# Optimization experiments

Hardware: AMD Instinct MI355X
Metric: run time of the kernel (lower is better)

Reference implementation:

```python
import jax, jax.numpy as jnp
import numpy as np

B, L, V, E, H, C, OUT = 128, 256, 50000, 300, 128, 4, 2
D = 2 * H  # features_size == sequence_max_len (required by the conv kernel width)
FS = (2, 3, 4, 5)


def _p(key, shape, s=0.05):
    return (jax.random.normal(key, shape) * s).astype(jnp.float32)


def setup_inputs() -> dict:
    key = jax.random.key(0)
    ks = jax.random.split(key, 32)
    emb = _p(ks[0], (V, E)).at[0].set(0.0)  # padding_idx=0
    inp = {
        'utterance': jax.random.randint(ks[1], (B, L), 1, V, dtype=jnp.int32),
        'seq_lengths': jnp.full((B,), L, dtype=jnp.int32),
        'emb': emb,
        'w_ih0': _p(ks[2], (2, 3 * H, E)), 'w_hh0': _p(ks[3], (2, 3 * H, H)),
        'b_ih0': _p(ks[4], (2, 3 * H)), 'b_hh0': _p(ks[5], (2, 3 * H)),
        'w_ih1': _p(ks[6], (2, 3 * H, 2 * H)), 'w_hh1': _p(ks[7], (2, 3 * H, H)),
        'b_ih1': _p(ks[8], (2, 3 * H)), 'b_hh1': _p(ks[9], (2, 3 * H)),
        'att_w': _p(ks[10], (C, D, D)), 'att_b': _p(ks[11], (C,)),
        'att_wv2': _p(ks[12], (C, D, D)), 'att_bv': _p(ks[13], (C, D)),
        'att_wv1': _p(ks[14], (C, D)),
        'fc_w': _p(ks[15], (OUT, sum(FS))), 'fc_b': _p(ks[16], (OUT,)),
    }
    for i, fs in enumerate(FS):
        inp[f'conv_w{i}'] = _p(ks[17 + 2 * i], (fs, C, fs, L))
        inp[f'conv_b{i}'] = _p(ks[18 + 2 * i], (fs,))
    return inp


def _gru_dir(x, w_ih, w_hh, b_ih, b_hh, reverse):
    # x: (B,T,in) -> (B,T,H); PyTorch GRU cell equations, eval mode (no dropout)
    gx = jnp.einsum('bti,gi->btg', x, w_ih) + b_ih  # (B,T,3H)

    def step(h, gxt):
        gh = h @ w_hh.T + b_hh
        xr, xz, xn = jnp.split(gxt, 3, axis=-1)
        hr, hz, hn = jnp.split(gh, 3, axis=-1)
        r = jax.nn.sigmoid(xr + hr)
        z = jax.nn.sigmoid(xz + hz)
        n = jnp.tanh(xn + r * hn)
        h = (1.0 - z) * n + z * h
        return h, h

    h0 = jnp.zeros((x.shape[0], w_hh.shape[1]), x.dtype)
    _, ys = jax.lax.scan(step, h0, jnp.swapaxes(gx, 0, 1), reverse=reverse)
    return jnp.swapaxes(ys, 0, 1)


def _bigru_layer(x, w_ih, w_hh, b_ih, b_hh):
    f = _gru_dir(x, w_ih[0], w_hh[0], b_ih[0], b_hh[0], False)
    b = _gru_dir(x, w_ih[1], w_hh[1], b_ih[1], b_hh[1], True)
    return jnp.concatenate([f, b], axis=-1)


def _forward(utterance, emb, w_ih0, w_hh0, b_ih0, b_hh0, w_ih1, w_hh1, b_ih1, b_hh1,
             att_w, att_b, att_wv2, att_bv, att_wv1, conv_params, fc_w, fc_b):
    x = emb[utterance]                                   # (B,L,E)
    x = _bigru_layer(x, w_ih0, w_hh0, b_ih0, b_hh0)      # (B,L,2H)
    x = _bigru_layer(x, w_ih1, w_hh1, b_ih1, b_hh1)      # (B,L,D)
    # --- AMCNN attention, vectorized over channels c ---
    mat = jnp.einsum('bld,cde->cble', x, att_w)          # mat_l per channel (C,B,L,D)
    # M_l[b,i,j] = <inputs[b,i], mat_l[b,j]> + b_l  (the torch tile/sum written as matmul)
    M = jnp.einsum('bid,cbjd->cbij', x, mat) + att_b[:, None, None, None]
    a = jax.nn.softmax(jnp.tanh(M).sum(axis=3), axis=2)  # scalar attention (C,B,L)
    g = jax.nn.sigmoid(jnp.einsum('bld,cde->cble', x, att_wv2) + att_bv[:, None, None, :])
    aa = jax.nn.softmax(jnp.einsum('cble,ce->cbl', g, att_wv1), axis=2)  # vector attn (C,B,L)
    new = jnp.einsum('cbl,bld->cbd', aa, x)              # weighted sum, broadcast over L
    Cf = a[..., None] * x[None] + new[:, :, None, :]     # (C,B,L,D)
    Cf = jnp.transpose(Cf, (1, 0, 2, 3))                 # (B,C,L,D)
    # --- conv blocks: Conv2d(k=(fs,L)) + ReLU + MaxPool((L-fs+1,1)) + Flatten ---
    pools = []
    for w, bi in conv_params:
        y = jax.lax.conv_general_dilated(Cf, w, (1, 1), 'VALID',
                                         dimension_numbers=('NCHW', 'OIHW', 'NCHW'))
        y = jax.nn.relu(y + bi[None, :, None, None])     # (B,fs,L-fs+1,1)
        pools.append(y.max(axis=(2, 3)))                 # (B,fs)
    feats = jnp.concatenate(pools, axis=-1)              # (B,sum(FS))
    return feats @ fc_w.T + fc_b                         # (B,OUT)


def reference(utterance, seq_lengths, emb, w_ih0, w_hh0, b_ih0, b_hh0,
              w_ih1, w_hh1, b_ih1, b_hh1, att_w, att_b, att_wv2, att_bv, att_wv1,
              conv_w0, conv_b0, conv_w1, conv_b1, conv_w2, conv_b2, conv_w3, conv_b3,
              fc_w, fc_b):
    # seq_lengths are all == L, so pack/pad_packed is an identity here
    conv_params = ((conv_w0, conv_b0), (conv_w1, conv_b1), (conv_w2, conv_b2), (conv_w3, conv_b3))
    return _forward(utterance, emb, w_ih0, w_hh0, b_ih0, b_hh0, w_ih1, w_hh1, b_ih1, b_hh1,
                    att_w, att_b, att_wv2, att_bv, att_wv1, conv_params, fc_w, fc_b)
```

## Files before the change

kernel.cpp:

```cpp
#include <hip/hip_runtime.h>
#include <hip/hip_bf16.h>
#include <hip/hip_fp16.h>

#define Bn  128
#define Ln  256
#define En  300
#define Hn  128
#define Cn  4
#define Dn  256
#define G3n 384
#define BLn (Bn * Ln)

typedef __hip_bfloat16 bf16;
typedef short s16x8 __attribute__((ext_vector_type(8)));
typedef float f32x4 __attribute__((ext_vector_type(4)));
typedef _Float16 h16x2 __attribute__((ext_vector_type(2)));

__device__ __forceinline__ float ldf(const float* p) { return *p; }
__device__ __forceinline__ float ldf(const bf16* p)  { return __bfloat162float(*p); }
__device__ __forceinline__ void stf(float* p, float v) { *p = v; }
__device__ __forceinline__ void stf(bf16* p, float v)  { *p = __float2bfloat16(v); }

__device__ __forceinline__ ushort f2bf(float f) {
    bf16 h = __float2bfloat16(f);
    return *reinterpret_cast<ushort*>(&h);
}
__device__ __forceinline__ float bfu(ushort x) {
    unsigned t = ((unsigned)x) << 16;
    return __builtin_bit_cast(float, t);
}

#if __has_builtin(__builtin_amdgcn_fdot2)
__device__ __forceinline__ float dot2f(h16x2 w, h16x2 h, float c) {
    return __builtin_amdgcn_fdot2(w, h, c, false);
}
#else
__device__ __forceinline__ float dot2f(h16x2 w, h16x2 h, float c) {
    return fmaf((float)w[0], (float)h[0], fmaf((float)w[1], (float)h[1], c));
}
#endif
#define BCH(x) __builtin_bit_cast(h16x2, x)

__device__ __forceinline__ float rdl(float v, int l) {
    return __builtin_bit_cast(float,
        __builtin_amdgcn_readlane(__builtin_bit_cast(int, v), l));
}

__device__ __forceinline__ float4 ld4f(const float* p) { return *(const float4*)p; }
__device__ __forceinline__ float4 ld4f(const bf16* p) {
    ushort4 u = *(const ushort4*)p;
    return make_float4(bfu(u.x), bfu(u.y), bfu(u.z), bfu(u.w));
}

template<class AT, class WTp, class OT, bool GATHER, int SM>
__global__ __launch_bounds__(256)
void gemm_mfma(const AT* __restrict__ A, const WTp* __restrict__ W,
               const float* __restrict__ bias, OT* __restrict__ Cout,
               const int* __restrict__ gidx, int M, int N, int K)
{
    __shared__ ushort Asm[128 * 40];
    __shared__ ushort Bsm[128 * 40];
    const int bm = blockIdx.y * 128, bn = blockIdx.x * 128;
    const int tid = threadIdx.x;
    const int lane = tid & 63, w = tid >> 6, wr = w >> 1, wc = w & 1;

    const AT* arow[4];
    const WTp* brow[4];
#pragma unroll
    for (int u = 0; u < 4; ++u) {
        const int idx = tid + u * 256;
        const int m = idx >> 3;
        arow[u] = A + (size_t)(GATHER ? gidx[bm + m] : (bm + m)) * K;
        brow[u] = W + (size_t)(bn + m) * K;
    }

    f32x4 acc[4][4] = {};
    const int nkt = (K + 31) >> 5;
    for (int kt = 0; kt < nkt; ++kt) {
        const int k0 = kt << 5;
#pragma unroll
        for (int u = 0; u < 4; ++u) {
            const int idx = tid + u * 256;
            const int m = idx >> 3, kq = idx & 7;
            const int kb = k0 + kq * 4;
            float4 v, q;
            if (kb + 4 <= K) {
                v = ld4f(arow[u] + kb);
                q = ld4f(brow[u] + kb);
            } else {
                v.x = kb + 0 < K ? ldf(&arow[u][kb + 0]) : 0.f;
                v.y = kb + 1 < K ? ldf(&arow[u][kb + 1]) : 0.f;
                v.z = kb + 2 < K ? ldf(&arow[u][kb + 2]) : 0.f;
                v.w = kb + 3 < K ? ldf(&arow[u][kb + 3]) : 0.f;
                q.x = kb + 0 < K ? ldf(&brow[u][kb + 0]) : 0.f;
                q.y = kb + 1 < K ? ldf(&brow[u][kb + 1]) : 0.f;
                q.z = kb + 2 < K ? ldf(&brow[u][kb + 2]) : 0.f;
                q.w = kb + 3 < K ? ldf(&brow[u][kb + 3]) : 0.f;
            }
            *(ushort4*)&Asm[m * 40 + kq * 4] =
                make_ushort4(f2bf(v.x), f2bf(v.y), f2bf(v.z), f2bf(v.w));
            *(ushort4*)&Bsm[m * 40 + kq * 4] =
                make_ushort4(f2bf(q.x), f2bf(q.y), f2bf(q.z), f2bf(q.w));
        }
        __syncthreads();
        s16x8 af[4], bfr[4];
#pragma unroll
        for (int t = 0; t < 4; ++t) {
            af[t]  = *(const s16x8*)&Asm[(wr * 64 + t * 16 + (lane & 15)) * 40 + (lane >> 4) * 8];
            bfr[t] = *(const s16x8*)&Bsm[(wc * 64 + t * 16 + (lane & 15)) * 40 + (lane >> 4) * 8];
        }
#pragma unroll
        for (int mf = 0; mf < 4; ++mf)
#pragma unroll
            for (int nf = 0; nf < 4; ++nf)
                acc[mf][nf] = __builtin_amdgcn_mfma_f32_16x16x32_bf16(
                    af[mf], bfr[nf], acc[mf][nf], 0, 0, 0);
        __syncthreads();
    }

#pragma unroll
    for (int mf = 0; mf < 4; ++mf)
#pragma unroll
        for (int nf = 0; nf < 4; ++nf) {
            const int col = bn + wc * 64 + nf * 16 + (lane & 15);
            const float bv_ = bias ? bias[col] : 0.f;
#pragma unroll
            for (int i = 0; i < 4; ++i) {
                const int row = bm + wr * 64 + mf * 16 + (lane >> 4) * 4 + i;
                const float v = acc[mf][nf][i] + bv_;
                if (SM == 1)
                    stf(&Cout[((size_t)(row >> 8) * N + col) * 256 + (row & 255)], v);
                else
                    stf(&Cout[(size_t)row * N + col], v);
            }
        }
}

__global__ __launch_bounds__(384, 1)
void gru_scan_v8(const bf16* __restrict__ gx, const float* __restrict__ w_hh,
                 const float* __restrict__ b_hh, bf16* __restrict__ out)
{
    const int b = blockIdx.x, dir = blockIdx.y;
    const int r = threadIdx.x;
    const int lane = r & 63;
    __shared__ __align__(16) ushort wl[384 * 136];
    __shared__ __align__(16) ushort hp16[128];
    __shared__ float h_sh[128];
    __shared__ float rs[128], zs[128], gxn[128], ghn[128];

    const float* wbase = w_hh + (size_t)dir * G3n * Hn;
    for (int idx = r; idx < G3n * 64; idx += 384) {
        const int row = idx >> 6, k2 = idx & 63;
        const float2 v = *(const float2*)(wbase + row * Hn + 2 * k2);
        h16x2 p; p[0] = (_Float16)v.x; p[1] = (_Float16)v.y;
        *(h16x2*)&wl[row * 136 + 2 * k2] = p;
    }
    if (r < 128) { hp16[r] = 0; h_sh[r] = 0.f; }
    const float bh = b_hh[dir * G3n + r];
    __syncthreads();

    const size_t g0 = (size_t)b * Ln * 768 + dir * G3n + r
                      + (dir ? (size_t)(Ln - 1) * 768 : 0);
    const long gstep = dir ? -768L : 768L;
    float gcur = ldf(&gx[g0]);
    float gnx  = ldf(&gx[g0 + gstep]);

    const ushort* wrow = &wl[r * 136];

    for (int s = 0; s < Ln; ++s) {
        const int t = dir ? (Ln - 1 - s) : s;
        float gn2 = 0.f;
        if (s + 2 < Ln) gn2 = ldf(&gx[g0 + (long)(s + 2) * gstep]);

        const float4 hown = *(const float4*)&hp16[(lane & 15) * 8];

        float a0 = 0.f, a1 = 0.f, a2 = 0.f, a3 = 0.f;
#pragma unroll
        for (int j = 0; j < 16; ++j) {
            const float4 wv = *(const float4*)&wrow[8 * j];
            a0 = dot2f(BCH(wv.x), BCH(rdl(hown.x, j)), a0);
            a1 = dot2f(BCH(wv.y), BCH(rdl(hown.y, j)), a1);
            a2 = dot2f(BCH(wv.z), BCH(rdl(hown.z, j)), a2);
            a3 = dot2f(BCH(wv.w), BCH(rdl(hown.w, j)), a3);
        }
        const float acc = (a0 + a1) + (a2 + a3) + bh;

        if (r < 128)      rs[r]       = 1.f / (1.f + expf(-(gcur + acc)));
        else if (r < 256) zs[r - 128] = 1.f / (1.f + expf(-(gcur + acc)));
        else { gxn[r - 256] = gcur; ghn[r - 256] = acc; }
        __syncthreads();

        if (r < 128) {
            const int j = r;
            const float nn = tanhf(gxn[j] + rs[j] * ghn[j]);
            const float hnew = (1.f - zs[j]) * nn + zs[j] * h_sh[j];
            h_sh[j] = hnew;
            const _Float16 hf = (_Float16)hnew;
            hp16[j] = __builtin_bit_cast(ushort, hf);
            out[((size_t)b * Ln + t) * Dn + dir * Hn + j] = __float2bfloat16(hnew);
        }
        __syncthreads();
        gcur = gnx; gnx = gn2;
    }
}

__global__ __launch_bounds__(256)
void attn_score_mfma(const bf16* __restrict__ x, const bf16* __restrict__ matc,
                     const float* __restrict__ attb, int c, float* __restrict__ sout)
{
    const int it = blockIdx.x, b = blockIdx.y;
    const bf16* A  = x    + ((size_t)b * 256 + it * 128) * 256;
    const bf16* Bm = matc + (size_t)b * 65536;
    __shared__ ushort Xs[128 * 40];
    __shared__ ushort Ms[128 * 40];
    const int tid = threadIdx.x, lane = tid & 63, w = tid >> 6;
    const float bc = attb[c];
    float psum[2][4] = {};

    for (int jt = 0; jt < 2; ++jt) {
        f32x4 acc[2][8] = {};
        for (int kt = 0; kt < 8; ++kt) {
            const int k0 = kt << 5;
#pragma unroll
            for (int u = 0; u < 2; ++u) {
                const int idx = tid + u * 256;
                const int m = idx >> 2, q = idx & 3;
                *(s16x8*)&Xs[m * 40 + q * 8] =
                    *(const s16x8*)&A[(size_t)m * 256 + k0 + q * 8];
                *(s16x8*)&Ms[m * 40 + q * 8] =
                    *(const s16x8*)&Bm[(size_t)(jt * 128 + m) * 256 + k0 + q * 8];
            }
            __syncthreads();
            s16x8 af[2], bfr[8];
#pragma unroll
            for (int t = 0; t < 2; ++t)
                af[t] = *(const s16x8*)&Xs[(w * 32 + t * 16 + (lane & 15)) * 40 + (lane >> 4) * 8];
#pragma unroll
            for (int t = 0; t < 8; ++t)
                bfr[t] = *(const s16x8*)&Ms[(t * 16 + (lane & 15)) * 40 + (lane >> 4) * 8];
#pragma unroll
            for (int mf = 0; mf < 2; ++mf)
#pragma unroll
                for (int nf = 0; nf < 8; ++nf)
                    acc[mf][nf] = __builtin_amdgcn_mfma_f32_16x16x32_bf16(
                        af[mf], bfr[nf], acc[mf][nf], 0, 0, 0);
            __syncthreads();
        }
#pragma unroll
        for (int mf = 0; mf < 2; ++mf)
#pragma unroll
            for (int nf = 0; nf < 8; ++nf)
#pragma unroll
                for (int i = 0; i < 4; ++i)
                    psum[mf][i] += tanhf(acc[mf][nf][i] + bc);
    }

#pragma unroll
    for (int mf = 0; mf < 2; ++mf)
#pragma unroll
        for (int i = 0; i < 4; ++i) {
            float v = psum[mf][i];
            v += __shfl_xor(v, 1); v += __shfl_xor(v, 2);
            v += __shfl_xor(v, 4); v += __shfl_xor(v, 8);
            if ((lane & 15) == 0)
                sout[b * 256 + it * 128 + w * 32 + mf * 16 + (lane >> 4) * 4 + i] = v;
        }
}

__global__ __launch_bounds__(256)
void gv_reduce(const bf16* __restrict__ gv, const float* __restrict__ bv,
               const float* __restrict__ wv1, float* __restrict__ al)
{
    const int row = blockIdx.x * 4 + (threadIdx.x >> 6);
    const int l = threadIdx.x & 63;
    const ushort4 u = *(const ushort4*)&gv[(size_t)row * 256 + l * 4];
    const float4 bb = *(const float4*)(bv + l * 4);
    const float4 w  = *(const float4*)(wv1 + l * 4);
    float s = w.x / (1.f + expf(-(bfu(u.x) + bb.x)))
            + w.y / (1.f + expf(-(bfu(u.y) + bb.y)))
            + w.z / (1.f + expf(-(bfu(u.z) + bb.z)))
            + w.w / (1.f + expf(-(bfu(u.w) + bb.w)));
#pragma unroll
    for (int m = 1; m < 64; m <<= 1) s += __shfl_xor(s, m);
    if (l == 0) al[row] = s;
}

__global__ void transpose256(const float* __restrict__ src, bf16* __restrict__ dst)
{
    const float* s = src + (size_t)blockIdx.x * 65536;
    bf16* d = dst + (size_t)blockIdx.x * 65536;
    __shared__ float t[32][33];
    const int tx = threadIdx.x & 31, ty8 = threadIdx.x >> 5;
    for (int bi = 0; bi < 8; ++bi)
        for (int bj = 0; bj < 8; ++bj) {
            __syncthreads();
            for (int r = ty8; r < 32; r += 8)
                t[r][tx] = s[(size_t)(bi * 32 + r) * 256 + bj * 32 + tx];
            __syncthreads();
            for (int r = ty8; r < 32; r += 8)
                stf(&d[(size_t)(bj * 32 + r) * 256 + bi * 32 + tx], t[tx][r]);
        }
}

__global__ void softmax256(const float* __restrict__ in, float* __restrict__ out)
{
    __shared__ float red[256];
    const int row = blockIdx.x, t = threadIdx.x;
    const float v = in[(size_t)row * 256 + t];
    red[t] = v; __syncthreads();
    for (int off = 128; off; off >>= 1) {
        if (t < off) red[t] = fmaxf(red[t], red[t + off]);
        __syncthreads();
    }
    const float mx = red[0]; __syncthreads();
    const float e = expf(v - mx);
    red[t] = e; __syncthreads();
    for (int off = 128; off; off >>= 1) {
        if (t < off) red[t] += red[t + off];
        __syncthreads();
    }
    out[(size_t)row * 256 + t] = e / red[0];
}

__global__ void weighted_sum_kernel(const float* __restrict__ aa,
                                    const bf16* __restrict__ x,
                                    float* __restrict__ outnew)
{
    const int b = blockIdx.x, c = blockIdx.y, d = threadIdx.x;
    __shared__ float w[Ln];
    w[d] = aa[((size_t)c * Bn + b) * Ln + d];
    __syncthreads();
    float acc = 0.f;
    for (int l = 0; l < Ln; ++l)
        acc += w[l] * ldf(&x[((size_t)b * Ln + l) * Dn + d]);
    outnew[((size_t)c * Bn + b) * Dn + d] = acc;
}

__global__ void wpack_fill(const float* __restrict__ w0, const float* __restrict__ w1,
                           const float* __restrict__ w2, const float* __restrict__ w3,
                           float* __restrict__ wp)
{
    const int f = blockIdx.x;
    if (f < 4) {
        const int cnt[4]  = {4096, 9216, 16384, 25600};
        const int boff[4] = {0, 4096, 13312, 29696};
        const float* src = f == 0 ? w0 : f == 1 ? w1 : f == 2 ? w2 : w3;
        for (int i = threadIdx.x; i < cnt[f]; i += blockDim.x)
            wp[boff[f] + i] = src[i];
    } else {
        for (int i = threadIdx.x; i < 65536 - 55296; i += blockDim.x)
            wp[55296 + i] = 0.f;
    }
}

__global__ __launch_bounds__(256)
void nwd_kernel(const float* __restrict__ nw, const float* __restrict__ wp,
                float* __restrict__ nwd)
{
    const int b = blockIdx.x;
    __shared__ float ns[4][256];
    for (int i = threadIdx.x; i < 1024; i += 256)
        ns[i >> 8][i & 255] = nw[((size_t)((i >> 8) * Bn + b) << 8) + (i & 255)];
    __syncthreads();
    const int row = threadIdx.x;
    if (row < 216) {
        int f, base;
        if (row < 16)       { f = 0; base = 0; }
        else if (row < 52)  { f = 1; base = 16; }
        else if (row < 116) { f = 2; base = 52; }
        else                { f = 3; base = 116; }
        const int fs = f + 2, local = row - base;
        const int c = (local / fs) & 3;
        const float* wr = wp + (size_t)row * 256;
        float acc = 0.f;
        for (int k = 0; k < 256; ++k) acc += ns[c][k] * wr[k];
        nwd[b * 256 + row] = acc;
    }
}

__global__ __launch_bounds__(256)
void conv_combine(const float* __restrict__ xwT, const float* __restrict__ a,
                  const float* __restrict__ nwd, const float* __restrict__ cb,
                  float* __restrict__ pool, int fs, int base, int poff)
{
    const int b = blockIdx.x, tid = threadIdx.x;
    __shared__ float ash[4][256];
    __shared__ float basev[5];
    __shared__ float red[256];
    for (int i = tid; i < 1024; i += 256)
        ash[i >> 8][i & 255] = a[((size_t)((i >> 8) * Bn + b) << 8) + (i & 255)];
    if (tid < fs) {
        float s = cb[tid];
        for (int c = 0; c < 4; ++c)
            for (int kh = 0; kh < fs; ++kh)
                s += nwd[b * 256 + base + (tid * 4 + c) * fs + kh];
        basev[tid] = s;
    }
    __syncthreads();
    const int ni = Ln - fs + 1;
    const float* xb = xwT + ((size_t)b << 16);
    for (int o = 0; o < fs; ++o) {
        float best = 0.f;
        if (tid < ni) {
            float acc = basev[o];
            for (int c = 0; c < 4; ++c)
                for (int kh = 0; kh < fs; ++kh) {
                    const int row = base + (o * 4 + c) * fs + kh;
                    acc += ash[c][tid + kh] * xb[(row << 8) + tid + kh];
                }
            best = fmaxf(acc, 0.f);
        }
        red[tid] = best; __syncthreads();
        for (int off = 128; off; off >>= 1) {
            if (tid < off) red[tid] = fmaxf(red[tid], red[tid + off]);
            __syncthreads();
        }
        if (tid == 0) pool[b * 14 + poff + o] = red[0];
        __syncthreads();
    }
}

__global__ void fc_kernel(const float* __restrict__ pool, const float* __restrict__ fw,
                          const float* __restrict__ fb, float* __restrict__ out)
{
    const int i = threadIdx.x;
    const int b = i >> 1, o = i & 1;
    float acc = fb[o];
#pragma unroll
    for (int f = 0; f < 14; ++f) acc += pool[b * 14 + f] * fw[o * 14 + f];
    out[i] = acc;
}

extern "C" void kernel_launch(void* const* d_in, const int* in_sizes, int n_in,
                              void* d_out, int out_size, void* d_ws, size_t ws_size,
                              hipStream_t stream)
{
    const int*   utt    = (const int*)  d_in[0];
    const float* emb    = (const float*)d_in[2];
    const float* w_ih0  = (const float*)d_in[3];
    const float* w_hh0  = (const float*)d_in[4];
    const float* b_ih0  = (const float*)d_in[5];
    const float* b_hh0  = (const float*)d_in[6];
    const float* w_ih1  = (const float*)d_in[7];
    const float* w_hh1  = (const float*)d_in[8];
    const float* b_ih1  = (const float*)d_in[9];
    const float* b_hh1  = (const float*)d_in[10];
    const float* att_w  = (const float*)d_in[11];
    const float* att_b  = (const float*)d_in[12];
    const float* att_wv2= (const float*)d_in[13];
    const float* att_bv = (const float*)d_in[14];
    const float* att_wv1= (const float*)d_in[15];
    const float* fc_w   = (const float*)d_in[16];
    const float* fc_b   = (const float*)d_in[17];
    const float* cw[4] = {(const float*)d_in[18], (const float*)d_in[20],
                          (const float*)d_in[22], (const float*)d_in[24]};
    const float* cb[4] = {(const float*)d_in[19], (const float*)d_in[21],
                          (const float*)d_in[23], (const float*)d_in[25]};

    float* ws = (float*)d_ws;
    bf16*  GX   = (bf16*)ws;
    bf16*  H1   = (bf16*)(ws + 12582912);
    bf16*  H2   = (bf16*)(ws + 12582912 + 4194304);
    bf16*  WT   = (bf16*)(ws + 20971520);
    float* WP   = ws + 20971520 + 131072;
    float* S    = WP + 65536;
    float* Aa   = S + 131072;
    float* AL   = Aa + 131072;
    float* AAa  = AL + 131072;
    float* NEW_ = AAa + 131072;
    float* NWD  = NEW_ + 131072;
    float* POOL = NWD + 32768;
    bf16*  MATc = H1;
    bf16*  GV   = (bf16*)ws;
    float* XWT  = ws;

    gemm_mfma<float, float, bf16, true, 0><<<dim3(6, 256), 256, 0, stream>>>(
        emb, w_ih0, b_ih0, GX, utt, BLn, 768, En);
    gru_scan_v8<<<dim3(Bn, 2), 384, 0, stream>>>(GX, w_hh0, b_hh0, H1);
    gemm_mfma<bf16, float, bf16, false, 0><<<dim3(6, 256), 256, 0, stream>>>(
        H1, w_ih1, b_ih1, GX, nullptr, BLn, 768, Dn);
    gru_scan_v8<<<dim3(Bn, 2), 384, 0, stream>>>(GX, w_hh1, b_hh1, H2);

    transpose256<<<4, 256, 0, stream>>>(att_w, WT);
    for (int c = 0; c < 4; ++c) {
        gemm_mfma<bf16, bf16, bf16, false, 0><<<dim3(2, 256), 256, 0, stream>>>(
            H2, WT + (size_t)c * 65536, nullptr, MATc, nullptr, BLn, Dn, Dn);
        attn_score_mfma<<<dim3(2, Bn), 256, 0, stream>>>(
            H2, MATc, att_b, c, S + (size_t)c * 32768);
    }
    softmax256<<<Cn * Bn, 256, 0, stream>>>(S, Aa);

    transpose256<<<4, 256, 0, stream>>>(att_wv2, WT);
    for (int c = 0; c < 4; ++c) {
        gemm_mfma<bf16, bf16, bf16, false, 0><<<dim3(2, 256), 256, 0, stream>>>(
            H2, WT + (size_t)c * 65536, nullptr, GV, nullptr, BLn, Dn, Dn);
        gv_reduce<<<BLn / 4, 256, 0, stream>>>(
            GV, att_bv + c * Dn, att_wv1 + c * Dn, AL + (size_t)c * BLn);
    }
    softmax256<<<Cn * Bn, 256, 0, stream>>>(AL, AAa);
    weighted_sum_kernel<<<dim3(Bn, Cn), 256, 0, stream>>>(AAa, H2, NEW_);

    wpack_fill<<<5, 256, 0, stream>>>(cw[0], cw[1], cw[2], cw[3], WP);
    gemm_mfma<bf16, float, float, false, 1><<<dim3(2, 256), 256, 0, stream>>>(
        H2, WP, nullptr, XWT, nullptr, BLn, Dn, Dn);
    nwd_kernel<<<Bn, 256, 0, stream>>>(NEW_, WP, NWD);

    const int baserow[4] = {0, 16, 52, 116};
    const int poff[4]    = {0, 2, 5, 9};
    for (int f = 0; f < 4; ++f)
        conv_combine<<<Bn, 256, 0, stream>>>(XWT, Aa, NWD, cb[f], POOL, f + 2, baserow[f], poff[f]);

    fc_kernel<<<1, 256, 0, stream>>>(POOL, fc_w, fc_b, (float*)d_out);
}
```

Baseline: 1.291 ms.

## Split GRU recurrent dot product across two thread halves and batch attention heads

The GRU scan kernel now runs 768 threads per block: each half computes half of the K=128 recurrent dot product from shared memory and the partial sums are combined through shared memory. This replaces the readlane broadcast of h and halves the serial dot-product chain per step, at the cost of an extra block-wide barrier per timestep. The attention stage fuses the four per-head GEMMs into one wider GEMM (N=1024), and each of attn_score and gv_reduce becomes a single launch with a head grid dimension, cutting the launch count and improving GEMM occupancy. This needs a larger workspace buffer for the combined output.

```diff
diff --git a/kernel.cpp b/kernel.cpp
--- a/kernel.cpp
+++ b/kernel.cpp
@@ -40,11 +40,6 @@
 }
 #endif
 #define BCH(x) __builtin_bit_cast(h16x2, x)
-
-__device__ __forceinline__ float rdl(float v, int l) {
-    return __builtin_bit_cast(float,
-        __builtin_amdgcn_readlane(__builtin_bit_cast(int, v), l));
-}
 
 __device__ __forceinline__ float4 ld4f(const float* p) { return *(const float4*)p; }
 __device__ __forceinline__ float4 ld4f(const bf16* p) {
@@ -136,81 +131,88 @@
         }
 }
 
-__global__ __launch_bounds__(384, 1)
-void gru_scan_v8(const bf16* __restrict__ gx, const float* __restrict__ w_hh,
+__global__ __launch_bounds__(768, 1)
+void gru_scan_v9(const bf16* __restrict__ gx, const float* __restrict__ w_hh,
                  const float* __restrict__ b_hh, bf16* __restrict__ out)
 {
     const int b = blockIdx.x, dir = blockIdx.y;
-    const int r = threadIdx.x;
-    const int lane = r & 63;
+    const int t = threadIdx.x;
+    const int half = t >= 384 ? 1 : 0;
+    const int r = t - 384 * half;
     __shared__ __align__(16) ushort wl[384 * 136];
     __shared__ __align__(16) ushort hp16[128];
     __shared__ float h_sh[128];
+    __shared__ float part[384];
     __shared__ float rs[128], zs[128], gxn[128], ghn[128];
 
     const float* wbase = w_hh + (size_t)dir * G3n * Hn;
-    for (int idx = r; idx < G3n * 64; idx += 384) {
+    for (int idx = t; idx < G3n * 64; idx += 768) {
         const int row = idx >> 6, k2 = idx & 63;
         const float2 v = *(const float2*)(wbase + row * Hn + 2 * k2);
         h16x2 p; p[0] = (_Float16)v.x; p[1] = (_Float16)v.y;
         *(h16x2*)&wl[row * 136 + 2 * k2] = p;
     }
-    if (r < 128) { hp16[r] = 0; h_sh[r] = 0.f; }
+    if (t < 128) { hp16[t] = 0; h_sh[t] = 0.f; }
     const float bh = b_hh[dir * G3n + r];
     __syncthreads();
 
     const size_t g0 = (size_t)b * Ln * 768 + dir * G3n + r
                       + (dir ? (size_t)(Ln - 1) * 768 : 0);
     const long gstep = dir ? -768L : 768L;
-    float gcur = ldf(&gx[g0]);
-    float gnx  = ldf(&gx[g0 + gstep]);
-
-    const ushort* wrow = &wl[r * 136];
+    float gcur = 0.f, gnx = 0.f;
+    if (!half) { gcur = ldf(&gx[g0]); gnx = ldf(&gx[g0 + gstep]); }
+
+    const ushort* wrow  = &wl[r * 136 + half * 64];
+    const ushort* hbase = &hp16[half * 64];
 
     for (int s = 0; s < Ln; ++s) {
-        const int t = dir ? (Ln - 1 - s) : s;
+        const int tt = dir ? (Ln - 1 - s) : s;
         float gn2 = 0.f;
-        if (s + 2 < Ln) gn2 = ldf(&gx[g0 + (long)(s + 2) * gstep]);
-
-        const float4 hown = *(const float4*)&hp16[(lane & 15) * 8];
+        if (!half && s + 2 < Ln) gn2 = ldf(&gx[g0 + (long)(s + 2) * gstep]);
 
         float a0 = 0.f, a1 = 0.f, a2 = 0.f, a3 = 0.f;
 #pragma unroll
-        for (int j = 0; j < 16; ++j) {
+        for (int j = 0; j < 8; ++j) {
             const float4 wv = *(const float4*)&wrow[8 * j];
-            a0 = dot2f(BCH(wv.x), BCH(rdl(hown.x, j)), a0);
-            a1 = dot2f(BCH(wv.y), BCH(rdl(hown.y, j)), a1);
-            a2 = dot2f(BCH(wv.z), BCH(rdl(hown.z, j)), a2);
-            a3 = dot2f(BCH(wv.w), BCH(rdl(hown.w, j)), a3);
-        }
-        const float acc = (a0 + a1) + (a2 + a3) + bh;
-
-        if (r < 128)      rs[r]       = 1.f / (1.f + expf(-(gcur + acc)));
-        else if (r < 256) zs[r - 128] = 1.f / (1.f + expf(-(gcur + acc)));
-        else { gxn[r - 256] = gcur; ghn[r - 256] = acc; }
-        __syncthreads();
-
-        if (r < 128) {
-            const int j = r;
+            const float4 hv = *(const float4*)&hbase[8 * j];
+            a0 = dot2f(BCH(wv.x), BCH(hv.x), a0);
+            a1 = dot2f(BCH(wv.y), BCH(hv.y), a1);
+            a2 = dot2f(BCH(wv.z), BCH(hv.z), a2);
+            a3 = dot2f(BCH(wv.w), BCH(hv.w), a3);
+        }
+        const float acc = (a0 + a1) + (a2 + a3);
+        if (half) part[r] = acc;
+        __syncthreads();
+
+        if (!half) {
+            const float tot = acc + part[r] + bh;
+            if (r < 128)      rs[r]       = 1.f / (1.f + expf(-(gcur + tot)));
+            else if (r < 256) zs[r - 128] = 1.f / (1.f + expf(-(gcur + tot)));
+            else { gxn[r - 256] = gcur; ghn[r - 256] = tot; }
+        }
+        __syncthreads();
+
+        if (t < 128) {
+            const int j = t;
             const float nn = tanhf(gxn[j] + rs[j] * ghn[j]);
             const float hnew = (1.f - zs[j]) * nn + zs[j] * h_sh[j];
             h_sh[j] = hnew;
             const _Float16 hf = (_Float16)hnew;
             hp16[j] = __builtin_bit_cast(ushort, hf);
-            out[((size_t)b * Ln + t) * Dn + dir * Hn + j] = __float2bfloat16(hnew);
-        }
-        __syncthreads();
-        gcur = gnx; gnx = gn2;
+            out[((size_t)b * Ln + tt) * Dn + dir * Hn + j] = __float2bfloat16(hnew);
+        }
+        __syncthreads();
+        if (!half) { gcur = gnx; gnx = gn2; }
     }
 }
 
 __global__ __launch_bounds__(256)
-void attn_score_mfma(const bf16* __restrict__ x, const bf16* __restrict__ matc,
-                     const float* __restrict__ attb, int c, float* __restrict__ sout)
-{
-    const int it = blockIdx.x, b = blockIdx.y;
-    const bf16* A  = x    + ((size_t)b * 256 + it * 128) * 256;
-    const bf16* Bm = matc + (size_t)b * 65536;
+void attn_score_mfma(const bf16* __restrict__ x, const bf16* __restrict__ matb,
+                     const float* __restrict__ attb, float* __restrict__ sout)
+{
+    const int it = blockIdx.x, b = blockIdx.y, c = blockIdx.z;
+    const bf16* A  = x + ((size_t)b * 256 + it * 128) * 256;
+    const bf16* Bm = matb + (size_t)b * 256 * 1024 + c * 256;
     __shared__ ushort Xs[128 * 40];
     __shared__ ushort Ms[128 * 40];
     const int tid = threadIdx.x, lane = tid & 63, w = tid >> 6;
@@ -228,7 +230,7 @@
                 *(s16x8*)&Xs[m * 40 + q * 8] =
                     *(const s16x8*)&A[(size_t)m * 256 + k0 + q * 8];
                 *(s16x8*)&Ms[m * 40 + q * 8] =
-                    *(const s16x8*)&Bm[(size_t)(jt * 128 + m) * 256 + k0 + q * 8];
+                    *(const s16x8*)&Bm[(size_t)(jt * 128 + m) * 1024 + k0 + q * 8];
             }
             __syncthreads();
             s16x8 af[2], bfr[8];
@@ -263,7 +265,7 @@
             v += __shfl_xor(v, 1); v += __shfl_xor(v, 2);
             v += __shfl_xor(v, 4); v += __shfl_xor(v, 8);
             if ((lane & 15) == 0)
-                sout[b * 256 + it * 128 + w * 32 + mf * 16 + (lane >> 4) * 4 + i] = v;
+                sout[(size_t)c * BLn + b * 256 + it * 128 + w * 32 + mf * 16 + (lane >> 4) * 4 + i] = v;
         }
 }
 
@@ -272,17 +274,18 @@
                const float* __restrict__ wv1, float* __restrict__ al)
 {
     const int row = blockIdx.x * 4 + (threadIdx.x >> 6);
+    const int c = blockIdx.y;
     const int l = threadIdx.x & 63;
-    const ushort4 u = *(const ushort4*)&gv[(size_t)row * 256 + l * 4];
-    const float4 bb = *(const float4*)(bv + l * 4);
-    const float4 w  = *(const float4*)(wv1 + l * 4);
+    const ushort4 u = *(const ushort4*)&gv[(size_t)row * 1024 + c * 256 + l * 4];
+    const float4 bb = *(const float4*)(bv + c * Dn + l * 4);
+    const float4 w  = *(const float4*)(wv1 + c * Dn + l * 4);
     float s = w.x / (1.f + expf(-(bfu(u.x) + bb.x)))
             + w.y / (1.f + expf(-(bfu(u.y) + bb.y)))
             + w.z / (1.f + expf(-(bfu(u.z) + bb.z)))
             + w.w / (1.f + expf(-(bfu(u.w) + bb.w)));
 #pragma unroll
     for (int m = 1; m < 64; m <<= 1) s += __shfl_xor(s, m);
-    if (l == 0) al[row] = s;
+    if (l == 0) al[(size_t)c * BLn + row] = s;
 }
 
 __global__ void transpose256(const float* __restrict__ src, bf16* __restrict__ dst)
@@ -460,7 +463,7 @@
     float* ws = (float*)d_ws;
     bf16*  GX   = (bf16*)ws;
     bf16*  H1   = (bf16*)(ws + 12582912);
-    bf16*  H2   = (bf16*)(ws + 12582912 + 4194304);
+    bf16*  H2   = (bf16*)(ws + 16777216);
     bf16*  WT   = (bf16*)(ws + 20971520);
     float* WP   = ws + 20971520 + 131072;
     float* S    = WP + 65536;
@@ -470,33 +473,26 @@
     float* NEW_ = AAa + 131072;
     float* NWD  = NEW_ + 131072;
     float* POOL = NWD + 32768;
-    bf16*  MATc = H1;
-    bf16*  GV   = (bf16*)ws;
+    bf16*  MATB = (bf16*)ws;
     float* XWT  = ws;
 
     gemm_mfma<float, float, bf16, true, 0><<<dim3(6, 256), 256, 0, stream>>>(
         emb, w_ih0, b_ih0, GX, utt, BLn, 768, En);
-    gru_scan_v8<<<dim3(Bn, 2), 384, 0, stream>>>(GX, w_hh0, b_hh0, H1);
+    gru_scan_v9<<<dim3(Bn, 2), 768, 0, stream>>>(GX, w_hh0, b_hh0, H1);
     gemm_mfma<bf16, float, bf16, false, 0><<<dim3(6, 256), 256, 0, stream>>>(
         H1, w_ih1, b_ih1, GX, nullptr, BLn, 768, Dn);
-    gru_scan_v8<<<dim3(Bn, 2), 384, 0, stream>>>(GX, w_hh1, b_hh1, H2);
+    gru_scan_v9<<<dim3(Bn, 2), 768, 0, stream>>>(GX, w_hh1, b_hh1, H2);
 
     transpose256<<<4, 256, 0, stream>>>(att_w, WT);
-    for (int c = 0; c < 4; ++c) {
-        gemm_mfma<bf16, bf16, bf16, false, 0><<<dim3(2, 256), 256, 0, stream>>>(
-            H2, WT + (size_t)c * 65536, nullptr, MATc, nullptr, BLn, Dn, Dn);
-        attn_score_mfma<<<dim3(2, Bn), 256, 0, stream>>>(
-            H2, MATc, att_b, c, S + (size_t)c * 32768);
-    }
+    gemm_mfma<bf16, bf16, bf16, false, 0><<<dim3(8, 256), 256, 0, stream>>>(
+        H2, WT, nullptr, MATB, nullptr, BLn, 1024, Dn);
+    attn_score_mfma<<<dim3(2, Bn, Cn), 256, 0, stream>>>(H2, MATB, att_b, S);
     softmax256<<<Cn * Bn, 256, 0, stream>>>(S, Aa);
 
     transpose256<<<4, 256, 0, stream>>>(att_wv2, WT);
-    for (int c = 0; c < 4; ++c) {
-        gemm_mfma<bf16, bf16, bf16, false, 0><<<dim3(2, 256), 256, 0, stream>>>(
-            H2, WT + (size_t)c * 65536, nullptr, GV, nullptr, BLn, Dn, Dn);
-        gv_reduce<<<BLn / 4, 256, 0, stream>>>(
-            GV, att_bv + c * Dn, att_wv1 + c * Dn, AL + (size_t)c * BLn);
-    }
+    gemm_mfma<bf16, bf16, bf16, false, 0><<<dim3(8, 256), 256, 0, stream>>>(
+        H2, WT, nullptr, MATB, nullptr, BLn, 1024, Dn);
+    gv_reduce<<<dim3(BLn / 4, Cn), 256, 0, stream>>>(MATB, att_bv, att_wv1, AL);
     softmax256<<<Cn * Bn, 256, 0, stream>>>(AL, AAa);
     weighted_sum_kernel<<<dim3(Bn, Cn), 256, 0, stream>>>(AAa, H2, NEW_);
 
```

Result: faster. 1.127 ms (-12.7%).
